# Performance work log

Hardware: AMD Instinct MI355X
Metric: run time of the kernel (lower is better)

## Reference

```python
import jax, jax.numpy as jnp
import numpy as np

B, T, C, H = 16, 2048, 1024, 64

def setup_inputs() -> dict:
    key = jax.random.key(0)
    kx, kq, kk, kv = jax.random.split(key, 4)
    s = 0.02
    return {
        "x": jax.random.normal(kx, (B, T, C), dtype=jnp.float32),
        "Wq": jax.random.normal(kq, (C, H), dtype=jnp.float32) * s,
        "Wk": jax.random.normal(kk, (C, H), dtype=jnp.float32) * s,
        "Wv": jax.random.normal(kv, (C, H), dtype=jnp.float32) * s,
    }

def reference(x, Wq, Wk, Wv):
    Bc, Tc, Cc = x.shape
    q = x @ Wq  # [B,T,H]
    k = x @ Wk  # [B,T,H]
    v = x @ Wv  # [B,T,H]
    # NOTE: original scales by n_embed^{-0.5} (C), not head_size^{-0.5}
    wei = jnp.einsum("bth,bsh->bts", q, k) * (Cc ** -0.5)  # [B,T,T]
    causal = jnp.tril(jnp.ones((Tc, Tc), dtype=bool))
    wei = jnp.where(causal, wei, -jnp.inf)
    wei = jax.nn.softmax(wei, axis=-1)
    # dropout is identity in eval mode
    out = jnp.einsum("bts,bsh->bth", wei, v)  # [B,T,H]
    return out
```

## Files before the change

### kernel.cpp

```cpp
#include <hip/hip_runtime.h>

typedef __attribute__((ext_vector_type(8))) short short8;
typedef __attribute__((ext_vector_type(4))) float float4v;

__device__ inline short f2bf(float f) {
    union { float f; unsigned int u; } c; c.f = f;
    unsigned int u = c.u;
    unsigned int r = (u + 0x7fffu + ((u >> 16) & 1u)) >> 16;
    return (short)r;
}

__device__ inline void gl2lds16(const short* g, short* l) {
    __builtin_amdgcn_global_load_lds(
        (const __attribute__((address_space(1))) unsigned int*)g,
        (__attribute__((address_space(3))) unsigned int*)l, 16, 0, 0);
}


__global__ __launch_bounds__(256) void wconv_kernel(
    const float* __restrict__ Wq, const float* __restrict__ Wk,
    const float* __restrict__ Wv, short* __restrict__ Wt_s)
{
    __shared__ short Ls[32 * 72];
    const int w  = blockIdx.x >> 5;
    const int c  = blockIdx.x & 31;
    const int k0 = c * 32;
    const float* W = (w == 0) ? Wq : (w == 1) ? Wk : Wv;
    const int tid = threadIdx.x;

    {
        int kk = tid >> 3;
        int c8 = (tid & 7) * 8;
        float4 v0 = *(const float4*)&W[(size_t)(k0 + kk) * 64 + c8];
        float4 v1 = *(const float4*)&W[(size_t)(k0 + kk) * 64 + c8 + 4];
        Ls[kk * 72 + c8 + 0] = f2bf(v0.x);
        Ls[kk * 72 + c8 + 1] = f2bf(v0.y);
        Ls[kk * 72 + c8 + 2] = f2bf(v0.z);
        Ls[kk * 72 + c8 + 3] = f2bf(v0.w);
        Ls[kk * 72 + c8 + 4] = f2bf(v1.x);
        Ls[kk * 72 + c8 + 5] = f2bf(v1.y);
        Ls[kk * 72 + c8 + 6] = f2bf(v1.z);
        Ls[kk * 72 + c8 + 7] = f2bf(v1.w);
    }
    __syncthreads();
    const int n = tid >> 2;
    const int g = tid & 3;
    short8 o;
#pragma unroll
    for (int j = 0; j < 8; j++) o[j] = Ls[(g * 8 + j) * 72 + n];
    const int gn = w * 64 + n;
    short* base = &Wt_s[((size_t)c * 192 + gn) * 32];
    *(short8*)&base[(g ^ (gn & 3)) * 8] = o;
}

__global__ __launch_bounds__(256, 4) void qkv_kernel(
    const float* __restrict__ x, const short* __restrict__ Wt_s,
    short* __restrict__ qo, short* __restrict__ k_s, short* __restrict__ vT_t)
{
    __shared__ short As[2][64 * 40];
    __shared__ short Bs[2][192 * 32];

    const int tid  = threadIdx.x;
    const int wave = tid >> 6, lane = tid & 63;
    const int quad = lane >> 4, l16 = lane & 15;
    const int m0   = blockIdx.x * 64;

    float4v acc[4][3];
#pragma unroll
    for (int mf = 0; mf < 4; mf++)
#pragma unroll
        for (int nt = 0; nt < 3; nt++) acc[mf][nt] = (float4v)0.0f;

    const int arow = tid >> 2;
    const int acol = (tid & 3) * 8;
    const float* ap = &x[(size_t)(m0 + arow) * 1024 + acol];
    const int lofs = lane * 8;

    {
        float4 x0 = *(const float4*)(ap);
        float4 x1 = *(const float4*)(ap + 4);
        const short* gsrc = Wt_s + ((size_t)wave * 48) * 32;
        short* ldst = &Bs[0][wave * 48 * 32];
#pragma unroll
        for (int i = 0; i < 3; i++)
            gl2lds16(gsrc + i * 512 + lofs, ldst + i * 512 + lofs);
        short8 av;
        av[0]=f2bf(x0.x); av[1]=f2bf(x0.y); av[2]=f2bf(x0.z); av[3]=f2bf(x0.w);
        av[4]=f2bf(x1.x); av[5]=f2bf(x1.y); av[6]=f2bf(x1.z); av[7]=f2bf(x1.w);
        *(short8*)&As[0][arow * 40 + acol] = av;
    }
    __syncthreads();

    for (int s = 0; s < 32; s++) {
        const int cb = s & 1, nb = cb ^ 1;
        const bool pf = (s + 1) < 32;
        float4 x0, x1;
        if (pf) {
            x0 = *(const float4*)(ap + (s + 1) * 32);
            x1 = *(const float4*)(ap + (s + 1) * 32 + 4);
            const short* gsrc = Wt_s + ((size_t)(s + 1) * 192 + wave * 48) * 32;
            short* ldst = &Bs[nb][wave * 48 * 32];
#pragma unroll
            for (int i = 0; i < 3; i++)
                gl2lds16(gsrc + i * 512 + lofs, ldst + i * 512 + lofs);
        }
        const short* Asc = As[cb];
        const short* Bsc = Bs[cb];
        short8 a0 = *(const short8*)&Asc[(     l16) * 40 + quad * 8];
        short8 a1 = *(const short8*)&Asc[(16 + l16) * 40 + quad * 8];
        short8 a2 = *(const short8*)&Asc[(32 + l16) * 40 + quad * 8];
        short8 a3 = *(const short8*)&Asc[(48 + l16) * 40 + quad * 8];
#pragma unroll
        for (int nt = 0; nt < 3; nt++) {
            int brow = wave * 48 + nt * 16 + l16;
            short8 bf = *(const short8*)&Bsc[brow * 32 + ((quad ^ (brow & 3)) * 8)];
            acc[0][nt] = __builtin_amdgcn_mfma_f32_16x16x32_bf16(a0, bf, acc[0][nt], 0, 0, 0);
            acc[1][nt] = __builtin_amdgcn_mfma_f32_16x16x32_bf16(a1, bf, acc[1][nt], 0, 0, 0);
            acc[2][nt] = __builtin_amdgcn_mfma_f32_16x16x32_bf16(a2, bf, acc[2][nt], 0, 0, 0);
            acc[3][nt] = __builtin_amdgcn_mfma_f32_16x16x32_bf16(a3, bf, acc[3][nt], 0, 0, 0);
        }
        if (pf) {
            short8 av;
            av[0]=f2bf(x0.x); av[1]=f2bf(x0.y); av[2]=f2bf(x0.z); av[3]=f2bf(x0.w);
            av[4]=f2bf(x1.x); av[5]=f2bf(x1.y); av[6]=f2bf(x1.z); av[7]=f2bf(x1.w);
            *(short8*)&As[nb][arow * 40 + acol] = av;
        }
        __syncthreads();
    }
#pragma unroll
    for (int mf = 0; mf < 4; mf++) {
#pragma unroll
        for (int nt = 0; nt < 3; nt++) {
            int g = wave * 48 + nt * 16 + l16;
#pragma unroll
            for (int r = 0; r < 4; r++) {
                int row = m0 + mf * 16 + quad * 4 + r;
                short val = f2bf(acc[mf][nt][r]);
                if (g < 64) {
                    qo[(size_t)row * 64 + g] = val;
                } else if (g < 128) {
                    int h = g - 64;
                    k_s[(size_t)row * 64 + (((h >> 3) ^ (row & 7)) * 8 + (h & 7))] = val;
                } else {
                    int h = g - 128;
                    int bb = row >> 11, tt = row & 2047;
                    int tc = tt >> 6, tl = tt & 63;
                    vT_t[(((size_t)bb * 32 + tc) * 64 + h) * 64 +
                         (((tl >> 3) ^ (h & 7)) * 8 + (tl & 7))] = val;
                }
            }
        }
    }
}

#define SCALE_LOG2E 0.04508422132f

__global__ __launch_bounds__(256) void attn_kernel(
    const short* __restrict__ q, const short* __restrict__ k_s,
    const short* __restrict__ vT_t, float* __restrict__ out)
{
    __shared__ short Ks[2][64 * 64];
    __shared__ short Vs[2][64 * 64];
    __shared__ short Ps[64 * 72];

    const int tid  = threadIdx.x;
    const int wave = tid >> 6, lane = tid & 63;
    const int quad = lane >> 4, l16 = lane & 15;

    int b, qt;
    if (blockIdx.x < 256) { b = blockIdx.x >> 4; qt = 16 + (blockIdx.x & 15); }
    else { int t2 = blockIdx.x - 256; b = t2 >> 4; qt = 15 - (t2 & 15); }

    const short* kb = k_s  + (size_t)b * 2048 * 64;
    const short* vb = vT_t + (size_t)b * 32 * 64 * 64;

    const short* qrow = q + ((size_t)b * 2048 + qt*64 + wave*16 + l16) * 64;
    short8 qf0 = *(const short8*)&qrow[quad*8];
    short8 qf1 = *(const short8*)&qrow[32 + quad*8];

    float4v oacc[4];
#pragma unroll
    for (int t = 0; t < 4; t++) oacc[t] = (float4v)0.0f;
    float l_i[4] = {0.f, 0.f, 0.f, 0.f};

    const int tg   = qt*64 + wave*16 + quad*4;
    const int jmax = qt;
    const int lofs = lane * 8;

    {
        const short* kg = kb + ((size_t)wave * 16) * 64;
        short* kl = &Ks[0][wave * 16 * 64];
        gl2lds16(kg +       lofs, kl +       lofs);
        gl2lds16(kg + 512 + lofs, kl + 512 + lofs);
        const short* vg = vb + ((size_t)wave * 16) * 64;
        short* vl = &Vs[0][wave * 16 * 64];
        gl2lds16(vg +       lofs, vl +       lofs);
        gl2lds16(vg + 512 + lofs, vl + 512 + lofs);
    }
    __syncthreads();

    int cur = 0;
    for (int j = 0; j <= jmax; j++) {
        const int nxt = cur ^ 1;
        if (j < jmax) {
            const short* kg = kb + ((size_t)(j + 1) * 64 + wave * 16) * 64;
            short* kl = &Ks[nxt][wave * 16 * 64];
            gl2lds16(kg +       lofs, kl +       lofs);
            gl2lds16(kg + 512 + lofs, kl + 512 + lofs);
            const short* vg = vb + ((size_t)(j + 1) * 64 + wave * 16) * 64;
            short* vl = &Vs[nxt][wave * 16 * 64];
            gl2lds16(vg +       lofs, vl +       lofs);
            gl2lds16(vg + 512 + lofs, vl + 512 + lofs);
        }
        const short* Ksc = Ks[cur];
        const short* Vsc = Vs[cur];

        float4v sacc[4];
#pragma unroll
        for (int t = 0; t < 4; t++) sacc[t] = (float4v)0.0f;
#pragma unroll
        for (int t = 0; t < 4; t++) {
            int brow = t*16 + l16;
            short8 b0 = *(const short8*)&Ksc[brow * 64 + ((    quad) ^ (brow & 7)) * 8];
            short8 b1 = *(const short8*)&Ksc[brow * 64 + ((4 + quad) ^ (brow & 7)) * 8];
            sacc[t] = __builtin_amdgcn_mfma_f32_16x16x32_bf16(qf0, b0, sacc[t], 0, 0, 0);
            sacc[t] = __builtin_amdgcn_mfma_f32_16x16x32_bf16(qf1, b1, sacc[t], 0, 0, 0);
        }
        if (j == jmax) {
#pragma unroll
            for (int t = 0; t < 4; t++) {
                int sg = j*64 + t*16 + l16;
#pragma unroll
                for (int r = 0; r < 4; r++) {
                    float p = exp2f(sacc[t][r] * SCALE_LOG2E);
                    if (sg > tg + r) p = 0.0f;
                    sacc[t][r] = p;
                    l_i[r] += p;
                }
            }
        } else {
#pragma unroll
            for (int t = 0; t < 4; t++)
#pragma unroll
                for (int r = 0; r < 4; r++) {
                    float p = exp2f(sacc[t][r] * SCALE_LOG2E);
                    sacc[t][r] = p;
                    l_i[r] += p;
                }
        }
#pragma unroll
        for (int t = 0; t < 4; t++)
#pragma unroll
            for (int r = 0; r < 4; r++)
                Ps[(wave*16 + quad*4 + r) * 72 + t*16 + l16] = f2bf(sacc[t][r]);
#pragma unroll
        for (int kc = 0; kc < 2; kc++) {
            short8 af = *(const short8*)&Ps[(wave*16 + l16) * 72 + kc*32 + quad*8];
#pragma unroll
            for (int t = 0; t < 4; t++) {
                int drow = t*16 + l16;
                short8 bf = *(const short8*)&Vsc[drow * 64 + ((kc*4 + quad) ^ (drow & 7)) * 8];
                oacc[t] = __builtin_amdgcn_mfma_f32_16x16x32_bf16(af, bf, oacc[t], 0, 0, 0);
            }
        }
        __syncthreads();
        cur = nxt;
    }
#pragma unroll
    for (int off = 1; off < 16; off <<= 1)
#pragma unroll
        for (int r = 0; r < 4; r++)
            l_i[r] += __shfl_xor(l_i[r], off, 64);
#pragma unroll
    for (int r = 0; r < 4; r++) {
        float inv = 1.0f / l_i[r];
        int row = qt*64 + wave*16 + quad*4 + r;
#pragma unroll
        for (int t = 0; t < 4; t++)
            out[((size_t)b * 2048 + row) * 64 + t*16 + l16] = oacc[t][r] * inv;
    }
}

extern "C" void kernel_launch(void* const* d_in, const int* in_sizes, int n_in,
                              void* d_out, int out_size, void* d_ws, size_t ws_size,
                              hipStream_t stream)
{
    const float* x  = (const float*)d_in[0];
    const float* Wq = (const float*)d_in[1];
    const float* Wk = (const float*)d_in[2];
    const float* Wv = (const float*)d_in[3];

    short* qw   = (short*)d_ws;
    short* ks   = qw + (size_t)32768 * 64;
    short* vTt  = ks + (size_t)32768 * 64;
    short* Wts  = vTt + (size_t)32768 * 64;
    float* out  = (float*)d_out;

    hipLaunchKernelGGL(wconv_kernel, dim3(96), dim3(256), 0, stream,
                       Wq, Wk, Wv, Wts);
    hipLaunchKernelGGL(qkv_kernel, dim3(512), dim3(256), 0, stream,
                       x, Wts, qw, ks, vTt);
    hipLaunchKernelGGL(attn_kernel, dim3(512), dim3(256), 0, stream,
                       qw, ks, vTt, out);
}
```

Before: 269.3 us.

## Make QKV projection waves independent with per-wave LDS buffers and no block barriers

The QKV projection kernel now gives each wave its own double-buffered LDS slice for the weight tile. Each wave loads its x rows straight into registers in MFMA fragment layout, so the shared A tile and all __syncthreads are gone. Ordering is handled with explicit vmcnt waits and a software-pipelined, manually unrolled loop. The row tile per block shrinks to 32, which doubles the grid to 1024 blocks. Every wave now reads the same x rows from global memory on its own, quadrupling x traffic, with the redundancy left to L1/L2 to absorb.

```diff
diff --git a/kernel.cpp b/kernel.cpp
--- a/kernel.cpp
+++ b/kernel.cpp
@@ -53,88 +53,87 @@
     *(short8*)&base[(g ^ (gn & 3)) * 8] = o;
 }
 
+#define QKV_STEP(BCUR, BNXT, XC0,XC1,XC2,XC3, XN0,XN1,XN2,XN3, SN, DOISS, WSTR) do { \
+    if (DOISS) {                                                                     \
+        const short* gsrc = Wt_s + ((size_t)(SN) * 192 + nc * 48) * 32 + lofs;       \
+        short* ldst = &Bs[wave][BNXT][lofs];                                         \
+        gl2lds16(gsrc,        ldst);                                                 \
+        gl2lds16(gsrc + 512,  ldst + 512);                                           \
+        gl2lds16(gsrc + 1024, ldst + 1024);                                          \
+        XN0 = *(const float4*)(xp0 + (SN) * 32);                                     \
+        XN1 = *(const float4*)(xp0 + (SN) * 32 + 4);                                 \
+        XN2 = *(const float4*)(xp1 + (SN) * 32);                                     \
+        XN3 = *(const float4*)(xp1 + (SN) * 32 + 4);                                 \
+    }                                                                                \
+    asm volatile(WSTR ::: "memory");                                                 \
+    __builtin_amdgcn_sched_barrier(0);                                               \
+    short8 af0, af1;                                                                 \
+    af0[0]=f2bf(XC0.x); af0[1]=f2bf(XC0.y); af0[2]=f2bf(XC0.z); af0[3]=f2bf(XC0.w);  \
+    af0[4]=f2bf(XC1.x); af0[5]=f2bf(XC1.y); af0[6]=f2bf(XC1.z); af0[7]=f2bf(XC1.w);  \
+    af1[0]=f2bf(XC2.x); af1[1]=f2bf(XC2.y); af1[2]=f2bf(XC2.z); af1[3]=f2bf(XC2.w);  \
+    af1[4]=f2bf(XC3.x); af1[5]=f2bf(XC3.y); af1[6]=f2bf(XC3.z); af1[7]=f2bf(XC3.w);  \
+    const short* Bc = &Bs[wave][BCUR][0];                                            \
+    _Pragma("unroll")                                                                \
+    for (int nt = 0; nt < 3; nt++) {                                                 \
+        short8 bf = *(const short8*)&Bc[(nt * 16 + l16) * 32 + swg];                 \
+        acc[0][nt] = __builtin_amdgcn_mfma_f32_16x16x32_bf16(af0, bf, acc[0][nt], 0, 0, 0); \
+        acc[1][nt] = __builtin_amdgcn_mfma_f32_16x16x32_bf16(af1, bf, acc[1][nt], 0, 0, 0); \
+    }                                                                                \
+} while (0)
+
 __global__ __launch_bounds__(256, 4) void qkv_kernel(
     const float* __restrict__ x, const short* __restrict__ Wt_s,
     short* __restrict__ qo, short* __restrict__ k_s, short* __restrict__ vT_t)
 {
-    __shared__ short As[2][64 * 40];
-    __shared__ short Bs[2][192 * 32];
+    __shared__ short Bs[4][2][1536];
 
     const int tid  = threadIdx.x;
     const int wave = tid >> 6, lane = tid & 63;
     const int quad = lane >> 4, l16 = lane & 15;
-    const int m0   = blockIdx.x * 64;
-
-    float4v acc[4][3];
-#pragma unroll
-    for (int mf = 0; mf < 4; mf++)
+    const int nc   = wave;
+    const int m0w  = blockIdx.x * 32;
+    const int lofs = lane * 8;
+    const int swg  = (quad ^ (l16 & 3)) * 8;
+
+    const float* xp0 = &x[(size_t)(m0w + l16) * 1024 + quad * 8];
+    const float* xp1 = xp0 + (size_t)16 * 1024;
+
+    float4v acc[2][3];
+#pragma unroll
+    for (int mf = 0; mf < 2; mf++)
 #pragma unroll
         for (int nt = 0; nt < 3; nt++) acc[mf][nt] = (float4v)0.0f;
 
-    const int arow = tid >> 2;
-    const int acol = (tid & 3) * 8;
-    const float* ap = &x[(size_t)(m0 + arow) * 1024 + acol];
-    const int lofs = lane * 8;
+    float4 xA0, xA1, xA2, xA3, xB0, xB1, xB2, xB3;
 
     {
-        float4 x0 = *(const float4*)(ap);
-        float4 x1 = *(const float4*)(ap + 4);
-        const short* gsrc = Wt_s + ((size_t)wave * 48) * 32;
-        short* ldst = &Bs[0][wave * 48 * 32];
-#pragma unroll
-        for (int i = 0; i < 3; i++)
-            gl2lds16(gsrc + i * 512 + lofs, ldst + i * 512 + lofs);
-        short8 av;
-        av[0]=f2bf(x0.x); av[1]=f2bf(x0.y); av[2]=f2bf(x0.z); av[3]=f2bf(x0.w);
-        av[4]=f2bf(x1.x); av[5]=f2bf(x1.y); av[6]=f2bf(x1.z); av[7]=f2bf(x1.w);
-        *(short8*)&As[0][arow * 40 + acol] = av;
-    }
-    __syncthreads();
-
-    for (int s = 0; s < 32; s++) {
-        const int cb = s & 1, nb = cb ^ 1;
-        const bool pf = (s + 1) < 32;
-        float4 x0, x1;
-        if (pf) {
-            x0 = *(const float4*)(ap + (s + 1) * 32);
-            x1 = *(const float4*)(ap + (s + 1) * 32 + 4);
-            const short* gsrc = Wt_s + ((size_t)(s + 1) * 192 + wave * 48) * 32;
-            short* ldst = &Bs[nb][wave * 48 * 32];
-#pragma unroll
-            for (int i = 0; i < 3; i++)
-                gl2lds16(gsrc + i * 512 + lofs, ldst + i * 512 + lofs);
-        }
-        const short* Asc = As[cb];
-        const short* Bsc = Bs[cb];
-        short8 a0 = *(const short8*)&Asc[(     l16) * 40 + quad * 8];
-        short8 a1 = *(const short8*)&Asc[(16 + l16) * 40 + quad * 8];
-        short8 a2 = *(const short8*)&Asc[(32 + l16) * 40 + quad * 8];
-        short8 a3 = *(const short8*)&Asc[(48 + l16) * 40 + quad * 8];
+        const short* gsrc = Wt_s + ((size_t)nc * 48) * 32 + lofs;
+        short* ldst = &Bs[wave][0][lofs];
+        gl2lds16(gsrc,        ldst);
+        gl2lds16(gsrc + 512,  ldst + 512);
+        gl2lds16(gsrc + 1024, ldst + 1024);
+        xA0 = *(const float4*)(xp0);
+        xA1 = *(const float4*)(xp0 + 4);
+        xA2 = *(const float4*)(xp1);
+        xA3 = *(const float4*)(xp1 + 4);
+    }
+
+    for (int sp = 0; sp < 15; sp++) {
+        const int s = sp * 2;
+        QKV_STEP(0, 1, xA0,xA1,xA2,xA3, xB0,xB1,xB2,xB3, s + 1, 1, "s_waitcnt vmcnt(7)");
+        QKV_STEP(1, 0, xB0,xB1,xB2,xB3, xA0,xA1,xA2,xA3, s + 2, 1, "s_waitcnt vmcnt(7)");
+    }
+    QKV_STEP(0, 1, xA0,xA1,xA2,xA3, xB0,xB1,xB2,xB3, 31, 1, "s_waitcnt vmcnt(7)");
+    QKV_STEP(1, 0, xB0,xB1,xB2,xB3, xA0,xA1,xA2,xA3, 32, 0, "s_waitcnt vmcnt(0)");
+
+#pragma unroll
+    for (int mf = 0; mf < 2; mf++) {
 #pragma unroll
         for (int nt = 0; nt < 3; nt++) {
-            int brow = wave * 48 + nt * 16 + l16;
-            short8 bf = *(const short8*)&Bsc[brow * 32 + ((quad ^ (brow & 3)) * 8)];
-            acc[0][nt] = __builtin_amdgcn_mfma_f32_16x16x32_bf16(a0, bf, acc[0][nt], 0, 0, 0);
-            acc[1][nt] = __builtin_amdgcn_mfma_f32_16x16x32_bf16(a1, bf, acc[1][nt], 0, 0, 0);
-            acc[2][nt] = __builtin_amdgcn_mfma_f32_16x16x32_bf16(a2, bf, acc[2][nt], 0, 0, 0);
-            acc[3][nt] = __builtin_amdgcn_mfma_f32_16x16x32_bf16(a3, bf, acc[3][nt], 0, 0, 0);
-        }
-        if (pf) {
-            short8 av;
-            av[0]=f2bf(x0.x); av[1]=f2bf(x0.y); av[2]=f2bf(x0.z); av[3]=f2bf(x0.w);
-            av[4]=f2bf(x1.x); av[5]=f2bf(x1.y); av[6]=f2bf(x1.z); av[7]=f2bf(x1.w);
-            *(short8*)&As[nb][arow * 40 + acol] = av;
-        }
-        __syncthreads();
-    }
-#pragma unroll
-    for (int mf = 0; mf < 4; mf++) {
-#pragma unroll
-        for (int nt = 0; nt < 3; nt++) {
-            int g = wave * 48 + nt * 16 + l16;
+            int g = nc * 48 + nt * 16 + l16;
 #pragma unroll
             for (int r = 0; r < 4; r++) {
-                int row = m0 + mf * 16 + quad * 4 + r;
+                int row = m0w + mf * 16 + quad * 4 + r;
                 short val = f2bf(acc[mf][nt][r]);
                 if (g < 64) {
                     qo[(size_t)row * 64 + g] = val;
@@ -298,7 +297,7 @@
 
     hipLaunchKernelGGL(wconv_kernel, dim3(96), dim3(256), 0, stream,
                        Wq, Wk, Wv, Wts);
-    hipLaunchKernelGGL(qkv_kernel, dim3(512), dim3(256), 0, stream,
+    hipLaunchKernelGGL(qkv_kernel, dim3(1024), dim3(256), 0, stream,
                        x, Wts, qw, ks, vTt);
     hipLaunchKernelGGL(attn_kernel, dim3(512), dim3(256), 0, stream,
                        qw, ks, vTt, out);
```

After: 288.8 us. 1.07x slower.
